# Optimization experiments

Measured on AMD Instinct MI355X. Metric: run time of the kernel, lower is better.

Reference implementation:

```python
import jax, jax.numpy as jnp
import numpy as np

B, P = 16, 1024
D_TIME, NUM_MODS = 8, 22
DIM_S = NUM_MODS + D_TIME + 1  # 31
PHI_W, N_HEADS, DP = 32, 4, 32
PSI_W, PSI_L, RHO_W = 64, 64, 64
SQRT_DP = float(np.sqrt(DP))


def setup_inputs() -> dict:
    key = jax.random.key(0)
    ks = jax.random.split(key, 16)
    rn = lambda k, shape: jax.random.normal(k, shape, jnp.float32) * 0.05
    return dict(
        times=jax.random.uniform(ks[0], (B, P), jnp.float32) * 48.0,
        values=jax.random.normal(ks[1], (B, P), jnp.float32),
        measurements=jax.random.randint(ks[2], (B, P), 0, NUM_MODS + 1),
        non_pad_mask=jnp.ones((B, P, 1), jnp.float32),
        W_psi1=rn(ks[3], (DIM_S, PSI_W)), b_psi1=jnp.zeros((PSI_W,), jnp.float32),
        W_psi2=rn(ks[4], (PSI_W, PSI_L)), b_psi2=jnp.zeros((PSI_L,), jnp.float32),
        W_key=rn(ks[5], (DIM_S + PSI_L, N_HEADS * DP)), b_key=jnp.zeros((N_HEADS * DP,), jnp.float32),
        query=rn(ks[6], (N_HEADS, DP)),
        W_phi1=rn(ks[7], (DIM_S, PHI_W)), b_phi1=jnp.zeros((PHI_W,), jnp.float32),
        W_phi2=rn(ks[8], (PHI_W, PHI_W)), b_phi2=jnp.zeros((PHI_W,), jnp.float32),
        W_rho1=rn(ks[9], (N_HEADS * PHI_W, RHO_W)), b_rho1=jnp.zeros((RHO_W,), jnp.float32),
        W_rho2=rn(ks[10], (RHO_W, RHO_W)), b_rho2=jnp.zeros((RHO_W,), jnp.float32),
    )


def _temporal_enc(times):
    i = np.arange(D_TIME)
    pos_vec = jnp.asarray(10000.0 ** (2.0 * (i // 2) / D_TIME), jnp.float32)
    ang = times[:, :, None] / pos_vec  # [B,P,d_time]
    return jnp.where(jnp.asarray(i % 2 == 0), jnp.sin(ang), jnp.cos(ang))


def reference(times, values, measurements, non_pad_mask,
              W_psi1, b_psi1, W_psi2, b_psi2, W_key, b_key, query,
              W_phi1, b_phi1, W_phi2, b_phi2, W_rho1, b_rho1, W_rho2, b_rho2):
    m = non_pad_mask  # [B,P,1]
    te = _temporal_enc(times)
    oh = jax.nn.one_hot(measurements, NUM_MODS + 1, dtype=jnp.float32)[:, :, 1:]
    x = jnp.concatenate([te, values[:, :, None], oh], axis=-1)  # [B,P,dim_s]

    # CumulativeSetAttentionLayer: psi MLP -> cumulative mean -> keys . query
    psi = jax.nn.relu(jax.nn.relu(x @ W_psi1 + b_psi1) @ W_psi2 + b_psi2)  # [B,P,psi_l]
    cum = jnp.cumsum(psi * m, axis=1) / jnp.cumsum(m, axis=1)
    keys = (jnp.concatenate([x, cum], axis=-1) @ W_key + b_key).reshape(B, P, N_HEADS, DP)
    pre = jnp.einsum('bpmd,md->bpm', keys, query) / SQRT_DP  # [B,P,m]

    # phi MLP
    phi = jax.nn.relu(jax.nn.relu(x @ W_phi1 + b_phi1) @ W_phi2 + b_phi2) * m  # [B,P,phi_w]

    # cumulative softmax weighting (online path)
    cmax = jax.lax.cummax(pre, axis=1)  # [B,P,m], running max for stability
    D = jnp.exp(pre[:, None, :, :] - cmax[:, :, None, :])  # [B,P,Q,m]
    causal = jnp.arange(P)[:, None] >= jnp.arange(P)[None, :]  # keep Q <= P
    D = D * causal[None, :, :, None]
    E = D.sum(axis=2)  # [B,P,m]
    agg = jnp.einsum('bpqm,bqd->bpmd', D, phi) / E[:, :, :, None]
    agg = (agg * m[:, :, :, None]).reshape(B, P, N_HEADS * PHI_W)

    # rho MLP (return_sequences)
    out = jax.nn.relu(jax.nn.relu(agg @ W_rho1 + b_rho1) @ W_rho2 + b_rho2) * m
    return out
```

## Files before the change

### kernel.cpp

```cpp
#include <hip/hip_runtime.h>
#include <hip/hip_bf16.h>

#define B_ 16
#define P_ 1024
#define T_ (B_*P_)
#define CH_ 32
#define CL_ (P_/CH_)

constexpr int OFF_A     = 16;
constexpr int OFF_WPSI1 = 400;
constexpr int OFF_BPSI1 = OFF_WPSI1 + 1984;
constexpr int OFF_WPSI2 = OFF_BPSI1 + 64;
constexpr int OFF_BPSI2 = OFF_WPSI2 + 4096;
constexpr int OFF_WPHI1 = OFF_BPSI2 + 64;
constexpr int OFF_BPHI1 = OFF_WPHI1 + 992;
constexpr int OFF_WPHI2 = OFF_BPHI1 + 32;
constexpr int OFF_BPHI2 = OFF_WPHI2 + 1024;
constexpr int OFF_WRHO1 = OFF_BPHI2 + 32;
constexpr int OFF_BRHO1 = OFF_WRHO1 + 8192;
constexpr int OFF_WRHO2 = OFF_BRHO1 + 64;
constexpr int OFF_BRHO2 = OFF_WRHO2 + 4096;
constexpr int OFF_PHI   = OFF_BRHO2 + 64;
constexpr int OFF_Z     = OFF_PHI   + T_*32;
constexpr int OFF_PREX  = OFF_Z     + T_*4;
constexpr int OFF_EXPW  = OFF_PREX  + T_*4;
constexpr int OFF_CE    = OFF_EXPW  + T_*4;
constexpr int OFF_CS    = OFF_CE    + 2048;

static __device__ __forceinline__ bool detect_f32(const void* mask_raw) {
  return ((*(const unsigned*)mask_raw) & 0xFFFFu) == 0u;
}
static __device__ __forceinline__ float ld_any(const void* src, int i, bool isf32) {
  if (isf32) return ((const float*)src)[i];
  return __bfloat162float(((const __hip_bfloat16*)src)[i]);
}

__global__ __launch_bounds__(256) void s01_prep(
    float* __restrict__ ws, const void* mask,
    const void* Wpsi1, const void* bpsi1, const void* Wpsi2, const void* bpsi2,
    const void* Wkey,  const void* bkey,  const void* query,
    const void* Wphi1, const void* bphi1, const void* Wphi2, const void* bphi2,
    const void* Wrho1, const void* brho1, const void* Wrho2, const void* brho2) {
  const bool isf32 = detect_f32(mask);
  if (blockIdx.x < 2) {
    const int gid = blockIdx.x * 256 + threadIdx.x;
    if (gid >= 384) return;
    const float inv_s = 0.17677669529663687f;
    const int h = gid & 3;
    const int j = gid >> 2;
    float s = 0.f;
    if (j < 95) {
      for (int d = 0; d < 32; ++d)
        s += ld_any(Wkey, j * 128 + h * 32 + d, isf32) * ld_any(query, h * 32 + d, isf32);
    } else {
      for (int d = 0; d < 32; ++d)
        s += ld_any(bkey, h * 32 + d, isf32) * ld_any(query, h * 32 + d, isf32);
    }
    ws[OFF_A + gid] = s * inv_s;
    return;
  }
  const int g  = (blockIdx.x - 2) * 256 + threadIdx.x;
  const int gs = (gridDim.x - 2) * 256;
  auto st = [&](int off, const void* src, int n) {
    for (int i = g; i < n; i += gs) ws[off + i] = ld_any(src, i, isf32);
  };
  st(OFF_WPSI1, Wpsi1, 1984); st(OFF_BPSI1, bpsi1, 64);
  st(OFF_WPSI2, Wpsi2, 4096); st(OFF_BPSI2, bpsi2, 64);
  st(OFF_WPHI1, Wphi1, 992);  st(OFF_BPHI1, bphi1, 32);
  st(OFF_WPHI2, Wphi2, 1024); st(OFF_BPHI2, bphi2, 32);
  st(OFF_WRHO1, Wrho1, 8192); st(OFF_BRHO1, brho1, 64);
  st(OFF_WRHO2, Wrho2, 4096); st(OFF_BRHO2, brho2, 64);
}

__global__ __launch_bounds__(256) void k1_token(float* __restrict__ ws,
                                                const int* __restrict__ measp,
                                                const void* __restrict__ times,
                                                const void* __restrict__ values,
                                                const void* __restrict__ mask) {
  __shared__ float sh1[4][64];
  __shared__ float sg1[4][32];
  const bool isf32 = detect_f32(mask);
  const int tid = threadIdx.x;
  const int wv  = __builtin_amdgcn_readfirstlane(tid >> 6);
  const int j   = tid & 63;
  const int t   = blockIdx.x * 4 + wv;

  const float tval = ld_any(times, t, isf32);
  const float vval = ld_any(values, t, isf32);
  const float mval = ld_any(mask, t, isf32);
  const int   meas = measp[t];
  const float sel  = (meas > 0) ? 1.f : 0.f;
  const int   mrow = (meas > 0) ? (8 + meas) : 0;

  float x[9];
  const float posv[4] = {1.f, 10.f, 100.f, 1000.f};
  #pragma unroll
  for (int k = 0; k < 4; ++k) {
    float s, c;
    __sincosf(tval / posv[k], &s, &c);
    x[2*k] = s; x[2*k+1] = c;
  }
  x[8] = vval;

  float h1 = ws[OFF_BPSI1 + j];
  #pragma unroll
  for (int i = 0; i < 9; ++i) h1 = fmaf(x[i], ws[OFF_WPSI1 + i * 64 + j], h1);
  h1 = fmaf(sel, ws[OFF_WPSI1 + mrow * 64 + j], h1);
  sh1[wv][j] = fmaxf(h1, 0.f);

  if (j < 32) {
    float g1 = ws[OFF_BPHI1 + j];
    #pragma unroll
    for (int i = 0; i < 9; ++i) g1 = fmaf(x[i], ws[OFF_WPHI1 + i * 32 + j], g1);
    g1 = fmaf(sel, ws[OFF_WPHI1 + mrow * 32 + j], g1);
    sg1[wv][j] = fmaxf(g1, 0.f);
  }
  __syncthreads();

  float h2 = ws[OFF_BPSI2 + j];
  #pragma unroll 8
  for (int i = 0; i < 64; ++i) h2 = fmaf(sh1[wv][i], ws[OFF_WPSI2 + i * 64 + j], h2);
  const float q = fmaxf(h2, 0.f) * mval;

  const float* a2 = ws + OFF_A + (31 + j) * 4;
  float z0 = q * a2[0], z1 = q * a2[1], z2 = q * a2[2], z3 = q * a2[3];
  #pragma unroll
  for (int off = 32; off; off >>= 1) {
    z0 += __shfl_xor(z0, off, 64);
    z1 += __shfl_xor(z1, off, 64);
    z2 += __shfl_xor(z2, off, 64);
    z3 += __shfl_xor(z3, off, 64);
  }
  if (j == 0) {
    float* zo = ws + OFF_Z + (size_t)t * 4;
    zo[0] = z0; zo[1] = z1; zo[2] = z2; zo[3] = z3;
  }

  if (j < 32) {
    float g2 = ws[OFF_BPHI2 + j];
    #pragma unroll 8
    for (int i = 0; i < 32; ++i) g2 = fmaf(sg1[wv][i], ws[OFF_WPHI2 + i * 32 + j], g2);
    ws[OFF_PHI + (size_t)t * 32 + j] = fmaxf(g2, 0.f) * mval;
  } else if (j < 36) {
    const int h = j - 32;
    float pr = ws[OFF_A + 380 + h];
    #pragma unroll
    for (int i = 0; i < 9; ++i) pr = fmaf(x[i], ws[OFF_A + i * 4 + h], pr);
    pr = fmaf(sel, ws[OFF_A + mrow * 4 + h], pr);
    ws[OFF_PREX + (size_t)t * 4 + h] = pr;
  }
}

__global__ __launch_bounds__(256) void k2_scanz(float* __restrict__ ws,
                                                const void* __restrict__ mask) {
  const int b    = blockIdx.x;
  const int tid  = threadIdx.x;
  const int lane = tid & 63;
  const int wv   = tid >> 6;
  const bool isf32 = detect_f32(mask);
  __shared__ float swt[4][5];
  __shared__ float smx[4][4];

  const float* zB = ws + OFF_Z + (size_t)b * P_ * 4;
  const int p0 = tid * 4;

  float lc[4], l0[4], l1[4], l2[4], l3[4];
  float c = 0.f, z0 = 0.f, z1 = 0.f, z2 = 0.f, z3 = 0.f;
  const float4* z4 = (const float4*)(zB + (size_t)p0 * 4);
  #pragma unroll
  for (int i = 0; i < 4; ++i) {
    const float4 zv = z4[i];
    c  += ld_any(mask, b * P_ + p0 + i, isf32);
    z0 += zv.x; z1 += zv.y; z2 += zv.z; z3 += zv.w;
    lc[i] = c; l0[i] = z0; l1[i] = z1; l2[i] = z2; l3[i] = z3;
  }

  float rc = c, r0 = z0, r1 = z1, r2 = z2, r3 = z3;
  #pragma unroll
  for (int off = 1; off < 64; off <<= 1) {
    const float uc = __shfl_up(rc, off, 64);
    const float u0 = __shfl_up(r0, off, 64);
    const float u1 = __shfl_up(r1, off, 64);
    const float u2 = __shfl_up(r2, off, 64);
    const float u3 = __shfl_up(r3, off, 64);
    if (lane >= off) { rc += uc; r0 += u0; r1 += u1; r2 += u2; r3 += u3; }
  }
  if (lane == 63) {
    swt[wv][0] = rc; swt[wv][1] = r0; swt[wv][2] = r1; swt[wv][3] = r2; swt[wv][4] = r3;
  }
  __syncthreads();
  #pragma unroll
  for (int w2 = 0; w2 < 3; ++w2) {
    if (wv > w2) {
      rc += swt[w2][0]; r0 += swt[w2][1]; r1 += swt[w2][2];
      r2 += swt[w2][3]; r3 += swt[w2][4];
    }
  }
  const float ec = rc - c, e0 = r0 - z0, e1 = r1 - z1, e2 = r2 - z2, e3 = r3 - z3;

  const float* px = ws + OFF_PREX + (size_t)b * P_ * 4;
  const float4* px4 = (const float4*)(px + (size_t)p0 * 4);
  float pre[4][4];
  float mx0 = -1e30f, mx1 = -1e30f, mx2 = -1e30f, mx3 = -1e30f;
  #pragma unroll
  for (int i = 0; i < 4; ++i) {
    const float inv = 1.f / (ec + lc[i]);
    const float4 pv = px4[i];
    pre[i][0] = pv.x + (e0 + l0[i]) * inv;
    pre[i][1] = pv.y + (e1 + l1[i]) * inv;
    pre[i][2] = pv.z + (e2 + l2[i]) * inv;
    pre[i][3] = pv.w + (e3 + l3[i]) * inv;
    mx0 = fmaxf(mx0, pre[i][0]); mx1 = fmaxf(mx1, pre[i][1]);
    mx2 = fmaxf(mx2, pre[i][2]); mx3 = fmaxf(mx3, pre[i][3]);
  }

  #pragma unroll
  for (int off = 32; off; off >>= 1) {
    mx0 = fmaxf(mx0, __shfl_xor(mx0, off, 64));
    mx1 = fmaxf(mx1, __shfl_xor(mx1, off, 64));
    mx2 = fmaxf(mx2, __shfl_xor(mx2, off, 64));
    mx3 = fmaxf(mx3, __shfl_xor(mx3, off, 64));
  }
  if (lane == 0) { smx[wv][0] = mx0; smx[wv][1] = mx1; smx[wv][2] = mx2; smx[wv][3] = mx3; }
  __syncthreads();
  const float M0 = fmaxf(fmaxf(smx[0][0], smx[1][0]), fmaxf(smx[2][0], smx[3][0]));
  const float M1 = fmaxf(fmaxf(smx[0][1], smx[1][1]), fmaxf(smx[2][1], smx[3][1]));
  const float M2 = fmaxf(fmaxf(smx[0][2], smx[1][2]), fmaxf(smx[2][2], smx[3][2]));
  const float M3 = fmaxf(fmaxf(smx[0][3], smx[1][3]), fmaxf(smx[2][3], smx[3][3]));

  float* eB = ws + OFF_EXPW + (size_t)b * P_ * 4;
  float4* e4 = (float4*)(eB + (size_t)p0 * 4);
  #pragma unroll
  for (int i = 0; i < 4; ++i) {
    float4 ev;
    ev.x = __expf(pre[i][0] - M0);
    ev.y = __expf(pre[i][1] - M1);
    ev.z = __expf(pre[i][2] - M2);
    ev.w = __expf(pre[i][3] - M3);
    e4[i] = ev;
  }
}

__global__ __launch_bounds__(128) void k4a_sums(float* __restrict__ ws) {
  const int ch = blockIdx.x, b = blockIdx.y;
  const int h = threadIdx.x >> 5, d = threadIdx.x & 31;
  const float* eB   = ws + OFF_EXPW + (size_t)b * P_ * 4;
  const float* phiB = ws + OFF_PHI  + (size_t)b * P_ * 32;

  float E = 0.f, S = 0.f;
  const int pbeg = ch * CL_;
  #pragma unroll 4
  for (int p = pbeg; p < pbeg + CL_; ++p) {
    const float e  = eB[p * 4 + h];
    const float ph = phiB[p * 32 + d];
    E += e;
    S = fmaf(e, ph, S);
  }
  const int base = (b * CH_ + ch) * 4 + h;
  if (d == 0) ws[OFF_CE + base] = E;
  ws[OFF_CS + base * 32 + d] = S;
}

__global__ __launch_bounds__(128) void k45_fused(float* __restrict__ ws,
                                                 const void* __restrict__ mask,
                                                 void* __restrict__ out) {
  __shared__ float sW1[128 * 64];
  __shared__ float sAgg[32][128];
  __shared__ float sH1[32][64];
  const int ch = blockIdx.x, b = blockIdx.y;
  const int tid = threadIdx.x;
  const int h = tid >> 5, d = tid & 31;
  const bool isf32 = detect_f32(mask);

  #pragma unroll 4
  for (int i = tid; i < 128 * 64; i += 128) sW1[i] = ws[OFF_WRHO1 + i];

  const float* eB   = ws + OFF_EXPW + (size_t)b * P_ * 4;
  const float* phiB = ws + OFF_PHI  + (size_t)b * P_ * 32;

  float E = 0.f, S = 0.f;
  for (int c2 = 0; c2 < ch; ++c2) {
    const int base2 = (b * CH_ + c2) * 4 + h;
    E += ws[OFF_CE + base2];
    S += ws[OFF_CS + base2 * 32 + d];
  }
  const int pbeg = ch * CL_;
  #pragma unroll 4
  for (int p = pbeg; p < pbeg + CL_; ++p) {
    const float e  = eB[p * 4 + h];
    const float ph = phiB[p * 32 + d];
    E += e;
    S = fmaf(e, ph, S);
    sAgg[p - pbeg][h * 32 + d] = (S / E) * ld_any(mask, b * P_ + p, isf32);
  }
  __syncthreads();

  const int j    = tid & 63;
  const int half = tid >> 6;
  const float b1 = ws[OFF_BRHO1 + j];
  float acc[16];
  #pragma unroll
  for (int k = 0; k < 16; ++k) acc[k] = b1;

  for (int i4 = 0; i4 < 32; ++i4) {
    const float w0 = sW1[(i4 * 4 + 0) * 64 + j];
    const float w1 = sW1[(i4 * 4 + 1) * 64 + j];
    const float w2 = sW1[(i4 * 4 + 2) * 64 + j];
    const float w3 = sW1[(i4 * 4 + 3) * 64 + j];
    #pragma unroll
    for (int k = 0; k < 16; ++k) {
      const float4 a = *(const float4*)&sAgg[half * 16 + k][i4 * 4];
      acc[k] = fmaf(a.w, w3, fmaf(a.z, w2, fmaf(a.y, w1, fmaf(a.x, w0, acc[k]))));
    }
  }
  #pragma unroll
  for (int k = 0; k < 16; ++k) sH1[half * 16 + k][j] = fmaxf(acc[k], 0.f);
  __syncthreads();

  const float b2 = ws[OFF_BRHO2 + j];
  float o[16];
  #pragma unroll
  for (int k = 0; k < 16; ++k) o[k] = b2;
  #pragma unroll 4
  for (int i = 0; i < 64; ++i) {
    const float w = ws[OFF_WRHO2 + i * 64 + j];
    #pragma unroll
    for (int k = 0; k < 16; ++k) o[k] = fmaf(sH1[half * 16 + k][i], w, o[k]);
  }

  const int t0 = b * P_ + pbeg + half * 16;
  #pragma unroll
  for (int k = 0; k < 16; ++k) {
    const float mv = ld_any(mask, t0 + k, isf32);
    const float v  = fmaxf(o[k], 0.f) * mv;
    if (isf32) {
      ((float*)out)[(size_t)(t0 + k) * 64 + j] = v;
    } else {
      ((__hip_bfloat16*)out)[(size_t)(t0 + k) * 64 + j] = __float2bfloat16(v);
    }
  }
}

extern "C" void kernel_launch(void* const* d_in, const int* in_sizes, int n_in,
                              void* d_out, int out_size, void* d_ws, size_t ws_size,
                              hipStream_t stream) {
  const int* meas = (const int*)d_in[2];
  const void* times = d_in[0];
  const void* values = d_in[1];
  const void* mask = d_in[3];
  float* ws = (float*)d_ws;

  s01_prep<<<34, 256, 0, stream>>>(ws, mask,
                                   d_in[4], d_in[5], d_in[6], d_in[7],
                                   d_in[8], d_in[9], d_in[10],
                                   d_in[11], d_in[12], d_in[13], d_in[14],
                                   d_in[15], d_in[16], d_in[17], d_in[18]);
  k1_token<<<T_/4, 256, 0, stream>>>(ws, meas, times, values, mask);
  k2_scanz<<<B_, 256, 0, stream>>>(ws, mask);
  k4a_sums<<<dim3(CH_, B_), 128, 0, stream>>>(ws);
  k45_fused<<<dim3(CH_, B_), 128, 0, stream>>>(ws, mask, d_out);
}
```

Measured before the change: 157.3 us.

## Fold weight-prep kernel into token and rho kernels with LDS-staged weights

Removes the separate prep launch: every k1_token block now loads the psi/phi weights into shared memory and recomputes the key·query projection itself. k45_fused moves to 256 threads, so half the block loads Wrho1 while the other half computes the cumulative aggregation, and rows per thread drop from 16 to 8. This saves one kernel launch and a workspace round trip. In exchange, each of the thousands of k1 blocks repeats about 8K weight loads plus the 384×32 dot products, and the larger shared-memory footprint may lower occupancy.

Measured after the change: 261.9 us. 66.5% more time.

```diff
diff --git a/kernel.cpp b/kernel.cpp
--- a/kernel.cpp
+++ b/kernel.cpp
@@ -35,55 +35,51 @@
   return __bfloat162float(((const __hip_bfloat16*)src)[i]);
 }
 
-__global__ __launch_bounds__(256) void s01_prep(
-    float* __restrict__ ws, const void* mask,
-    const void* Wpsi1, const void* bpsi1, const void* Wpsi2, const void* bpsi2,
-    const void* Wkey,  const void* bkey,  const void* query,
-    const void* Wphi1, const void* bphi1, const void* Wphi2, const void* bphi2,
-    const void* Wrho1, const void* brho1, const void* Wrho2, const void* brho2) {
+__global__ __launch_bounds__(256) void k1_token(float* __restrict__ ws,
+    const int* __restrict__ measp, const void* __restrict__ times,
+    const void* __restrict__ values, const void* __restrict__ mask,
+    const void* __restrict__ Wpsi1, const void* __restrict__ bpsi1,
+    const void* __restrict__ Wpsi2, const void* __restrict__ bpsi2,
+    const void* __restrict__ Wkey,  const void* __restrict__ bkey,
+    const void* __restrict__ query,
+    const void* __restrict__ Wphi1, const void* __restrict__ bphi1,
+    const void* __restrict__ Wphi2, const void* __restrict__ bphi2) {
+  __shared__ float sWpsi1[1984], sBpsi1[64], sWpsi2[4096], sBpsi2[64];
+  __shared__ float sWphi1[992],  sBphi1[32], sWphi2[1024], sBphi2[32];
+  __shared__ float sA[384];
+  __shared__ float sA2T[256];
+  __shared__ float sh1[4][64], sg1[4][32];
   const bool isf32 = detect_f32(mask);
-  if (blockIdx.x < 2) {
-    const int gid = blockIdx.x * 256 + threadIdx.x;
-    if (gid >= 384) return;
-    const float inv_s = 0.17677669529663687f;
-    const int h = gid & 3;
-    const int j = gid >> 2;
+  const int tid = threadIdx.x;
+
+  for (int i = tid; i < 1984; i += 256) sWpsi1[i] = ld_any(Wpsi1, i, isf32);
+  for (int i = tid; i < 4096; i += 256) sWpsi2[i] = ld_any(Wpsi2, i, isf32);
+  for (int i = tid; i < 992;  i += 256) sWphi1[i] = ld_any(Wphi1, i, isf32);
+  for (int i = tid; i < 1024; i += 256) sWphi2[i] = ld_any(Wphi2, i, isf32);
+  if      (tid < 64)  sBpsi1[tid]       = ld_any(bpsi1, tid,       isf32);
+  else if (tid < 128) sBpsi2[tid - 64]  = ld_any(bpsi2, tid - 64,  isf32);
+  else if (tid < 160) sBphi1[tid - 128] = ld_any(bphi1, tid - 128, isf32);
+  else if (tid < 192) sBphi2[tid - 160] = ld_any(bphi2, tid - 160, isf32);
+
+  for (int g = tid; g < 384; g += 256) {
+    const int h = g & 3, jj = g >> 2;
     float s = 0.f;
-    if (j < 95) {
+    if (jj < 95) {
       for (int d = 0; d < 32; ++d)
-        s += ld_any(Wkey, j * 128 + h * 32 + d, isf32) * ld_any(query, h * 32 + d, isf32);
+        s += ld_any(Wkey, jj * 128 + h * 32 + d, isf32) * ld_any(query, h * 32 + d, isf32);
     } else {
       for (int d = 0; d < 32; ++d)
         s += ld_any(bkey, h * 32 + d, isf32) * ld_any(query, h * 32 + d, isf32);
     }
-    ws[OFF_A + gid] = s * inv_s;
-    return;
-  }
-  const int g  = (blockIdx.x - 2) * 256 + threadIdx.x;
-  const int gs = (gridDim.x - 2) * 256;
-  auto st = [&](int off, const void* src, int n) {
-    for (int i = g; i < n; i += gs) ws[off + i] = ld_any(src, i, isf32);
-  };
-  st(OFF_WPSI1, Wpsi1, 1984); st(OFF_BPSI1, bpsi1, 64);
-  st(OFF_WPSI2, Wpsi2, 4096); st(OFF_BPSI2, bpsi2, 64);
-  st(OFF_WPHI1, Wphi1, 992);  st(OFF_BPHI1, bphi1, 32);
-  st(OFF_WPHI2, Wphi2, 1024); st(OFF_BPHI2, bphi2, 32);
-  st(OFF_WRHO1, Wrho1, 8192); st(OFF_BRHO1, brho1, 64);
-  st(OFF_WRHO2, Wrho2, 4096); st(OFF_BRHO2, brho2, 64);
-}
-
-__global__ __launch_bounds__(256) void k1_token(float* __restrict__ ws,
-                                                const int* __restrict__ measp,
-                                                const void* __restrict__ times,
-                                                const void* __restrict__ values,
-                                                const void* __restrict__ mask) {
-  __shared__ float sh1[4][64];
-  __shared__ float sg1[4][32];
-  const bool isf32 = detect_f32(mask);
-  const int tid = threadIdx.x;
-  const int wv  = __builtin_amdgcn_readfirstlane(tid >> 6);
-  const int j   = tid & 63;
-  const int t   = blockIdx.x * 4 + wv;
+    s *= 0.17677669529663687f;
+    sA[g] = s;
+    if (jj >= 31 && jj < 95) sA2T[h * 64 + (jj - 31)] = s;
+  }
+  __syncthreads();
+
+  const int wv = __builtin_amdgcn_readfirstlane(tid >> 6);
+  const int j  = tid & 63;
+  const int t  = blockIdx.x * 4 + wv;
 
   const float tval = ld_any(times, t, isf32);
   const float vval = ld_any(values, t, isf32);
@@ -102,28 +98,28 @@
   }
   x[8] = vval;
 
-  float h1 = ws[OFF_BPSI1 + j];
-  #pragma unroll
-  for (int i = 0; i < 9; ++i) h1 = fmaf(x[i], ws[OFF_WPSI1 + i * 64 + j], h1);
-  h1 = fmaf(sel, ws[OFF_WPSI1 + mrow * 64 + j], h1);
+  float h1 = sBpsi1[j];
+  #pragma unroll
+  for (int i = 0; i < 9; ++i) h1 = fmaf(x[i], sWpsi1[i * 64 + j], h1);
+  h1 = fmaf(sel, sWpsi1[mrow * 64 + j], h1);
   sh1[wv][j] = fmaxf(h1, 0.f);
 
   if (j < 32) {
-    float g1 = ws[OFF_BPHI1 + j];
+    float g1 = sBphi1[j];
     #pragma unroll
-    for (int i = 0; i < 9; ++i) g1 = fmaf(x[i], ws[OFF_WPHI1 + i * 32 + j], g1);
-    g1 = fmaf(sel, ws[OFF_WPHI1 + mrow * 32 + j], g1);
+    for (int i = 0; i < 9; ++i) g1 = fmaf(x[i], sWphi1[i * 32 + j], g1);
+    g1 = fmaf(sel, sWphi1[mrow * 32 + j], g1);
     sg1[wv][j] = fmaxf(g1, 0.f);
   }
   __syncthreads();
 
-  float h2 = ws[OFF_BPSI2 + j];
+  float h2 = sBpsi2[j];
   #pragma unroll 8
-  for (int i = 0; i < 64; ++i) h2 = fmaf(sh1[wv][i], ws[OFF_WPSI2 + i * 64 + j], h2);
+  for (int i = 0; i < 64; ++i) h2 = fmaf(sh1[wv][i], sWpsi2[i * 64 + j], h2);
   const float q = fmaxf(h2, 0.f) * mval;
 
-  const float* a2 = ws + OFF_A + (31 + j) * 4;
-  float z0 = q * a2[0], z1 = q * a2[1], z2 = q * a2[2], z3 = q * a2[3];
+  float z0 = q * sA2T[0 * 64 + j], z1 = q * sA2T[1 * 64 + j];
+  float z2 = q * sA2T[2 * 64 + j], z3 = q * sA2T[3 * 64 + j];
   #pragma unroll
   for (int off = 32; off; off >>= 1) {
     z0 += __shfl_xor(z0, off, 64);
@@ -137,16 +133,16 @@
   }
 
   if (j < 32) {
-    float g2 = ws[OFF_BPHI2 + j];
+    float g2 = sBphi2[j];
     #pragma unroll 8
-    for (int i = 0; i < 32; ++i) g2 = fmaf(sg1[wv][i], ws[OFF_WPHI2 + i * 32 + j], g2);
+    for (int i = 0; i < 32; ++i) g2 = fmaf(sg1[wv][i], sWphi2[i * 32 + j], g2);
     ws[OFF_PHI + (size_t)t * 32 + j] = fmaxf(g2, 0.f) * mval;
   } else if (j < 36) {
     const int h = j - 32;
-    float pr = ws[OFF_A + 380 + h];
+    float pr = sA[380 + h];
     #pragma unroll
-    for (int i = 0; i < 9; ++i) pr = fmaf(x[i], ws[OFF_A + i * 4 + h], pr);
-    pr = fmaf(sel, ws[OFF_A + mrow * 4 + h], pr);
+    for (int i = 0; i < 9; ++i) pr = fmaf(x[i], sA[i * 4 + h], pr);
+    pr = fmaf(sel, sA[mrow * 4 + h], pr);
     ws[OFF_PREX + (size_t)t * 4 + h] = pr;
   }
 }
@@ -261,76 +257,87 @@
   ws[OFF_CS + base * 32 + d] = S;
 }
 
-__global__ __launch_bounds__(128) void k45_fused(float* __restrict__ ws,
-                                                 const void* __restrict__ mask,
-                                                 void* __restrict__ out) {
-  __shared__ float sW1[128 * 64];
+__global__ __launch_bounds__(256) void k45_fused(float* __restrict__ ws,
+    const void* __restrict__ mask,
+    const void* __restrict__ Wrho1, const void* __restrict__ brho1,
+    const void* __restrict__ Wrho2, const void* __restrict__ brho2,
+    void* __restrict__ out) {
+  __shared__ float sW1[8192];
   __shared__ float sAgg[32][128];
   __shared__ float sH1[32][64];
   const int ch = blockIdx.x, b = blockIdx.y;
   const int tid = threadIdx.x;
-  const int h = tid >> 5, d = tid & 31;
   const bool isf32 = detect_f32(mask);
-
-  #pragma unroll 4
-  for (int i = tid; i < 128 * 64; i += 128) sW1[i] = ws[OFF_WRHO1 + i];
-
-  const float* eB   = ws + OFF_EXPW + (size_t)b * P_ * 4;
-  const float* phiB = ws + OFF_PHI  + (size_t)b * P_ * 32;
-
-  float E = 0.f, S = 0.f;
-  for (int c2 = 0; c2 < ch; ++c2) {
-    const int base2 = (b * CH_ + c2) * 4 + h;
-    E += ws[OFF_CE + base2];
-    S += ws[OFF_CS + base2 * 32 + d];
-  }
   const int pbeg = ch * CL_;
-  #pragma unroll 4
-  for (int p = pbeg; p < pbeg + CL_; ++p) {
-    const float e  = eB[p * 4 + h];
-    const float ph = phiB[p * 32 + d];
-    E += e;
-    S = fmaf(e, ph, S);
-    sAgg[p - pbeg][h * 32 + d] = (S / E) * ld_any(mask, b * P_ + p, isf32);
-  }
-  __syncthreads();
-
-  const int j    = tid & 63;
-  const int half = tid >> 6;
-  const float b1 = ws[OFF_BRHO1 + j];
-  float acc[16];
-  #pragma unroll
-  for (int k = 0; k < 16; ++k) acc[k] = b1;
-
+
+  if (tid < 128) {
+    const int h = tid >> 5, d = tid & 31;
+    const float* eB   = ws + OFF_EXPW + (size_t)b * P_ * 4;
+    const float* phiB = ws + OFF_PHI  + (size_t)b * P_ * 32;
+    float E = 0.f, S = 0.f;
+    for (int c2 = 0; c2 < ch; ++c2) {
+      const int base2 = (b * CH_ + c2) * 4 + h;
+      E += ws[OFF_CE + base2];
+      S += ws[OFF_CS + base2 * 32 + d];
+    }
+    #pragma unroll 4
+    for (int p = pbeg; p < pbeg + CL_; ++p) {
+      const float e  = eB[p * 4 + h];
+      const float ph = phiB[p * 32 + d];
+      E += e;
+      S = fmaf(e, ph, S);
+      sAgg[p - pbeg][h * 32 + d] = (S / E) * ld_any(mask, b * P_ + p, isf32);
+    }
+  } else {
+    for (int i = tid - 128; i < 8192; i += 128) sW1[i] = ld_any(Wrho1, i, isf32);
+  }
+  __syncthreads();
+
+  const int j = tid & 63, qw = tid >> 6;
+  const float b1 = ld_any(brho1, j, isf32);
+  float acc[8];
+  #pragma unroll
+  for (int k = 0; k < 8; ++k) acc[k] = b1;
   for (int i4 = 0; i4 < 32; ++i4) {
     const float w0 = sW1[(i4 * 4 + 0) * 64 + j];
     const float w1 = sW1[(i4 * 4 + 1) * 64 + j];
     const float w2 = sW1[(i4 * 4 + 2) * 64 + j];
     const float w3 = sW1[(i4 * 4 + 3) * 64 + j];
     #pragma unroll
-    for (int k = 0; k < 16; ++k) {
-      const float4 a = *(const float4*)&sAgg[half * 16 + k][i4 * 4];
+    for (int k = 0; k < 8; ++k) {
+      const float4 a = *(const float4*)&sAgg[qw * 8 + k][i4 * 4];
       acc[k] = fmaf(a.w, w3, fmaf(a.z, w2, fmaf(a.y, w1, fmaf(a.x, w0, acc[k]))));
     }
   }
   #pragma unroll
-  for (int k = 0; k < 16; ++k) sH1[half * 16 + k][j] = fmaxf(acc[k], 0.f);
-  __syncthreads();
-
-  const float b2 = ws[OFF_BRHO2 + j];
-  float o[16];
-  #pragma unroll
-  for (int k = 0; k < 16; ++k) o[k] = b2;
-  #pragma unroll 4
-  for (int i = 0; i < 64; ++i) {
-    const float w = ws[OFF_WRHO2 + i * 64 + j];
-    #pragma unroll
-    for (int k = 0; k < 16; ++k) o[k] = fmaf(sH1[half * 16 + k][i], w, o[k]);
-  }
-
-  const int t0 = b * P_ + pbeg + half * 16;
-  #pragma unroll
-  for (int k = 0; k < 16; ++k) {
+  for (int k = 0; k < 8; ++k) sH1[qw * 8 + k][j] = fmaxf(acc[k], 0.f);
+  __syncthreads();
+
+  const float b2 = ld_any(brho2, j, isf32);
+  float o[8];
+  #pragma unroll
+  for (int k = 0; k < 8; ++k) o[k] = b2;
+  if (isf32) {
+    const float* W2 = (const float*)Wrho2;
+    #pragma unroll 4
+    for (int i = 0; i < 64; ++i) {
+      const float w = W2[i * 64 + j];
+      #pragma unroll
+      for (int k = 0; k < 8; ++k) o[k] = fmaf(sH1[qw * 8 + k][i], w, o[k]);
+    }
+  } else {
+    const __hip_bfloat16* W2 = (const __hip_bfloat16*)Wrho2;
+    #pragma unroll 4
+    for (int i = 0; i < 64; ++i) {
+      const float w = __bfloat162float(W2[i * 64 + j]);
+      #pragma unroll
+      for (int k = 0; k < 8; ++k) o[k] = fmaf(sH1[qw * 8 + k][i], w, o[k]);
+    }
+  }
+
+  const int t0 = b * P_ + pbeg + qw * 8;
+  #pragma unroll
+  for (int k = 0; k < 8; ++k) {
     const float mv = ld_any(mask, t0 + k, isf32);
     const float v  = fmaxf(o[k], 0.f) * mv;
     if (isf32) {
@@ -350,13 +357,13 @@
   const void* mask = d_in[3];
   float* ws = (float*)d_ws;
 
-  s01_prep<<<34, 256, 0, stream>>>(ws, mask,
-                                   d_in[4], d_in[5], d_in[6], d_in[7],
-                                   d_in[8], d_in[9], d_in[10],
-                                   d_in[11], d_in[12], d_in[13], d_in[14],
-                                   d_in[15], d_in[16], d_in[17], d_in[18]);
-  k1_token<<<T_/4, 256, 0, stream>>>(ws, meas, times, values, mask);
+  k1_token<<<T_/4, 256, 0, stream>>>(ws, meas, times, values, mask,
+                                     d_in[4], d_in[5], d_in[6], d_in[7],
+                                     d_in[8], d_in[9], d_in[10],
+                                     d_in[11], d_in[12], d_in[13], d_in[14]);
   k2_scanz<<<B_, 256, 0, stream>>>(ws, mask);
   k4a_sums<<<dim3(CH_, B_), 128, 0, stream>>>(ws);
-  k45_fused<<<dim3(CH_, B_), 128, 0, stream>>>(ws, mask, d_out);
-}
+  k45_fused<<<dim3(CH_, B_), 256, 0, stream>>>(ws, mask,
+                                               d_in[15], d_in[16], d_in[17], d_in[18],
+                                               d_out);
+}
```
